# Kernel optimization log

Hardware: AMD Instinct MI355X
Metric: run time of the kernel (lower is better)

## Reference

```python
import jax, jax.numpy as jnp
import numpy as np

N, E = 100000, 800000
DIN, DH, DOUT = 128, 64, 16


def _glorot_linear(k, din, dout):
    s = 1.0 / np.sqrt(din)
    return jax.random.uniform(k, (din, dout), jnp.float32, -s, s)


def setup_inputs() -> dict:
    key = jax.random.key(0)
    ks = jax.random.split(key, 6)
    x = jax.random.normal(ks[0], (N, DIN), jnp.float32)
    edge_index = jax.random.randint(ks[1], (2, E), 0, N, dtype=jnp.int64)
    edge_attr = jax.random.uniform(ks[2], (E,), jnp.float32)  # positive edge weights
    W1 = _glorot_linear(ks[3], DIN, DH)
    b1 = jnp.zeros((DH,), jnp.float32)
    W2 = _glorot_linear(ks[4], DH, DH)
    b2 = jnp.zeros((DH,), jnp.float32)
    W3 = _glorot_linear(ks[5], DH, DOUT)
    b3 = jnp.zeros((DOUT,), jnp.float32)
    return {"x": x, "edge_index": edge_index, "edge_attr": edge_attr,
            "W1": W1, "b1": b1, "W2": W2, "b2": b2, "W3": W3, "b3": b3}


def gcn_conv(x, W, b, src, dst, ew, n):
    """PyG GCNConv: linear transform, add self-loops (weight 1), symmetric
    degree normalization, scatter-add aggregation (source_to_target), bias."""
    h = x @ W                                   # [N, dout]
    deg = jax.ops.segment_sum(ew, dst, num_segments=n) + 1.0  # +1 for self-loop
    dinv = jax.lax.rsqrt(deg)                   # deg >= 1 always
    norm = dinv[src] * ew * dinv[dst]           # [E]
    agg = jax.ops.segment_sum(h[src] * norm[:, None], dst, num_segments=n)
    # self-loop contribution: h[i] * dinv[i]^2
    return agg + h * (dinv * dinv)[:, None] + b


def reference(x, edge_index, edge_attr, W1, b1, W2, b2, W3, b3):
    src, dst = edge_index[0], edge_index[1]
    n = x.shape[0]
    h = jax.nn.relu(gcn_conv(x, W1, b1, src, dst, edge_attr, n))
    # dropout is identity in eval mode
    h = jax.nn.relu(gcn_conv(h, W2, b2, src, dst, edge_attr, n))
    h = gcn_conv(h, W3, b3, src, dst, edge_attr, n)
    return jax.nn.log_softmax(h, axis=1)
```

## Files before the change

### kernel.cpp

```cpp
#include <hip/hip_runtime.h>
#include <hip/hip_bf16.h>
#include <math.h>

#define DIN 128
#define DH 64
#define DOUT_ 16
#define SL 32
#define BSH 9
#define NBMAX 256
#define CAP 5120
#define CH 2048

typedef long long ll;
typedef __attribute__((ext_vector_type(8))) short bf16x8;
typedef __attribute__((ext_vector_type(4))) float f32x4;

__device__ inline ushort f2bf(float f) {
    unsigned u = __float_as_uint(f);
    u += 0x7FFF + ((u >> 16) & 1);
    return (ushort)(u >> 16);
}
__device__ inline float bf2f(ushort s) { return __uint_as_float(((unsigned)s) << 16); }

__global__ __launch_bounds__(256) void bin_and_gemm(const int* __restrict__ src,
                                                    const int* __restrict__ dst,
                                                    const float* __restrict__ ew,
                                                    int* __restrict__ gcur,
                                                    int2* __restrict__ bins, int E,
                                                    const float* __restrict__ X,
                                                    const float* __restrict__ W,
                                                    ushort* __restrict__ H, int N,
                                                    int FB) {
    __shared__ int hist[NBMAX];
    __shared__ int curb[NBMAX];
    __shared__ int baseb[NBMAX];
    __shared__ __align__(16) ushort Wt[DIN * DH];

    const int tid = threadIdx.x;

    if (blockIdx.x < FB) {
        for (int i = tid; i < NBMAX; i += 256) { hist[i] = 0; curb[i] = 0; }
        __syncthreads();
        const int e0 = blockIdx.x * CH;
        const int ecnt = min(E - e0, CH);
        for (int r = tid; r < ecnt; r += 256)
            atomicAdd(&hist[dst[e0 + r] >> BSH], 1);
        __syncthreads();
        for (int b = tid; b < NBMAX; b += 256)
            baseb[b] = hist[b] ? atomicAdd(&gcur[b], hist[b]) : 0;
        __syncthreads();
        for (int r = tid; r < ecnt; r += 256) {
            int e = e0 + r;
            int d = dst[e];
            int b = d >> BSH;
            int off = atomicAdd(&curb[b], 1);
            int pos = baseb[b] + off;
            if (pos < CAP)
                bins[(ll)b * CAP + pos] =
                    make_int2(src[e] | ((d & ((1 << BSH) - 1)) << 20), __float_as_int(ew[e]));
        }
        return;
    }

    const int bid = blockIdx.x - FB;
    for (int f = tid; f < DIN * DH; f += 256) {
        int k = f / DH, c = f % DH;
        Wt[((k >> 3) * DH + c) * 8 + (k & 7)] = f2bf(W[f]);
    }
    __syncthreads();

    const int wave = tid >> 6;
    const int lane = tid & 63;
    const int rowTile = bid * 64 + wave * 16;
    const int arow = rowTile + (lane & 15);
    const int kgrp = lane >> 4;

    f32x4 acc[DH / 16];
    #pragma unroll
    for (int cf = 0; cf < DH / 16; cf++) acc[cf] = (f32x4){0.f, 0.f, 0.f, 0.f};

    #pragma unroll
    for (int ks = 0; ks < DIN / 32; ks++) {
        const int k0 = ks * 32 + kgrp * 8;
        bf16x8 a = {0, 0, 0, 0, 0, 0, 0, 0};
        if (arow < N) {
            const float* xp = X + (ll)arow * DIN + k0;
            float4 f0 = ((const float4*)xp)[0];
            float4 f1 = ((const float4*)xp)[1];
            a[0] = (short)f2bf(f0.x); a[1] = (short)f2bf(f0.y);
            a[2] = (short)f2bf(f0.z); a[3] = (short)f2bf(f0.w);
            a[4] = (short)f2bf(f1.x); a[5] = (short)f2bf(f1.y);
            a[6] = (short)f2bf(f1.z); a[7] = (short)f2bf(f1.w);
        }
        #pragma unroll
        for (int cf = 0; cf < DH / 16; cf++) {
            bf16x8 b = *(const bf16x8*)&Wt[(((k0 >> 3) * DH) + cf * 16 + (lane & 15)) * 8];
            acc[cf] = __builtin_amdgcn_mfma_f32_16x16x32_bf16(a, b, acc[cf], 0, 0, 0);
        }
    }

    const int rbase = rowTile + kgrp * 4;
    #pragma unroll
    for (int cf = 0; cf < DH / 16; cf++) {
        #pragma unroll
        for (int r = 0; r < 4; r++) {
            int row = rbase + r;
            if (row < N)
                H[(ll)row * DH + cf * 16 + (lane & 15)] = f2bf(acc[cf][r]);
        }
    }
}

__global__ __launch_bounds__(256) void debin(const int2* __restrict__ bins,
                                             const int* __restrict__ gcur,
                                             int2* __restrict__ pair, int* __restrict__ cnt,
                                             float* __restrict__ dinv, int N) {
    __shared__ int cl[1 << BSH];
    __shared__ float wsum[1 << BSH];
    const int tid = threadIdx.x;
    for (int i = tid; i < (1 << BSH); i += 256) { cl[i] = 0; wsum[i] = 0.f; }
    __syncthreads();

    const int b = blockIdx.x;
    const int nbase = b << BSH;
    const int m = min(gcur[b], CAP);
    for (int i = tid; i < m; i += 256) {
        int2 t = bins[(ll)b * CAP + i];
        int dlo = t.x >> 20;
        int s = t.x & 0xFFFFF;
        int slot = atomicAdd(&cl[dlo], 1);
        if (slot < SL) pair[(ll)(nbase + dlo) * SL + slot] = make_int2(s, t.y);
        atomicAdd(&wsum[dlo], __int_as_float(t.y));
    }
    __syncthreads();
    for (int i = tid; i < (1 << BSH); i += 256) {
        int node = nbase + i;
        if (node < N) {
            cnt[node] = min(cl[i], SL);
            dinv[node] = rsqrtf(wsum[i] + 1.0f);
        }
    }
}

template <int NC, bool SRC_DINV>
__global__ __launch_bounds__(256) void fused_gg(const ushort* __restrict__ h,
                                                const int2* __restrict__ pair,
                                                const int* __restrict__ cnt,
                                                const float* __restrict__ dinv,
                                                const float* __restrict__ bias,
                                                const float* __restrict__ W,
                                                ushort* __restrict__ Hout, int N) {
    __shared__ __align__(16) ushort Wt[64 * NC];
    __shared__ __align__(16) ushort Hs[64][72];

    for (int f = threadIdx.x; f < 64 * NC; f += 256) {
        int k = f / NC, c = f % NC;
        Wt[((k >> 3) * NC + c) * 8 + (k & 7)] = f2bf(W[f]);
    }

    const int tid = threadIdx.x;
    const int grp = tid >> 4;
    const int l16 = tid & 15;
    const ushort4* h4 = (const ushort4*)h;

    #pragma unroll
    for (int pass = 0; pass < 4; pass++) {
        int nl = pass * 16 + grp;
        int node = blockIdx.x * 64 + nl;
        float4 acc = make_float4(0.f, 0.f, 0.f, 0.f);
        float di = 0.f;
        float hx = 0.f, hy = 0.f, hz = 0.f, hw = 0.f;
        float4 bv = make_float4(0.f, 0.f, 0.f, 0.f);
        if (node < N) {
            int deg = min(cnt[node], SL);
            const int2* p = pair + (ll)node * SL;
            int e = 0;
            for (; e + 1 < deg; e += 2) {
                int2 p0 = p[e];
                int2 p1 = p[e + 1];
                ushort4 a0 = h4[(ll)p0.x * 16 + l16];
                ushort4 a1 = h4[(ll)p1.x * 16 + l16];
                float w0 = __int_as_float(p0.y);
                float w1 = __int_as_float(p1.y);
                if (SRC_DINV) { w0 *= dinv[p0.x]; w1 *= dinv[p1.x]; }
                acc.x += bf2f(a0.x) * w0 + bf2f(a1.x) * w1;
                acc.y += bf2f(a0.y) * w0 + bf2f(a1.y) * w1;
                acc.z += bf2f(a0.z) * w0 + bf2f(a1.z) * w1;
                acc.w += bf2f(a0.w) * w0 + bf2f(a1.w) * w1;
            }
            if (e < deg) {
                int2 pp = p[e];
                ushort4 a0 = h4[(ll)pp.x * 16 + l16];
                float w = __int_as_float(pp.y);
                if (SRC_DINV) w *= dinv[pp.x];
                acc.x += bf2f(a0.x) * w;
                acc.y += bf2f(a0.y) * w;
                acc.z += bf2f(a0.z) * w;
                acc.w += bf2f(a0.w) * w;
            }
            di = dinv[node];
            ushort4 hs = h4[(ll)node * 16 + l16];
            float sf = SRC_DINV ? di : 1.0f;
            hx = bf2f(hs.x) * sf; hy = bf2f(hs.y) * sf;
            hz = bf2f(hs.z) * sf; hw = bf2f(hs.w) * sf;
            bv = ((const float4*)bias)[l16];
        }
        float rx = fmaxf(di * (acc.x + hx) + bv.x, 0.f);
        float ry = fmaxf(di * (acc.y + hy) + bv.y, 0.f);
        float rz = fmaxf(di * (acc.z + hz) + bv.z, 0.f);
        float rw = fmaxf(di * (acc.w + hw) + bv.w, 0.f);
        *(ushort4*)&Hs[nl][l16 * 4] = make_ushort4(f2bf(rx), f2bf(ry), f2bf(rz), f2bf(rw));
    }
    __syncthreads();

    const int wave = tid >> 6;
    const int lane = tid & 63;
    const int kgrp = lane >> 4;
    f32x4 acc2[NC / 16];
    #pragma unroll
    for (int cf = 0; cf < NC / 16; cf++) acc2[cf] = (f32x4){0.f, 0.f, 0.f, 0.f};

    #pragma unroll
    for (int ks = 0; ks < 2; ks++) {
        const int k0 = ks * 32 + kgrp * 8;
        bf16x8 a = *(const bf16x8*)&Hs[wave * 16 + (lane & 15)][k0];
        #pragma unroll
        for (int cf = 0; cf < NC / 16; cf++) {
            bf16x8 b = *(const bf16x8*)&Wt[(((k0 >> 3) * NC) + cf * 16 + (lane & 15)) * 8];
            acc2[cf] = __builtin_amdgcn_mfma_f32_16x16x32_bf16(a, b, acc2[cf], 0, 0, 0);
        }
    }

    const int rbase = blockIdx.x * 64 + wave * 16 + kgrp * 4;
    float dsc[4];
    #pragma unroll
    for (int r = 0; r < 4; r++) dsc[r] = (rbase + r < N) ? dinv[rbase + r] : 1.0f;
    #pragma unroll
    for (int cf = 0; cf < NC / 16; cf++) {
        #pragma unroll
        for (int r = 0; r < 4; r++) {
            int row = rbase + r;
            if (row < N)
                Hout[(ll)row * NC + cf * 16 + (lane & 15)] = f2bf(acc2[cf][r] * dsc[r]);
        }
    }
}

__global__ __launch_bounds__(256) void gather16_final(const ushort* __restrict__ h3,
                                                      const int2* __restrict__ pair,
                                                      const int* __restrict__ cnt,
                                                      const float* __restrict__ dinv,
                                                      const float* __restrict__ b3,
                                                      float* __restrict__ out, int N) {
    int node = blockIdx.x * 32 + (threadIdx.x >> 3);
    int lane = threadIdx.x & 7;
    if (node >= N) return;
    int deg = min(cnt[node], SL);
    const int2* p = pair + (ll)node * SL;

    const ushort2* h2 = (const ushort2*)h3;
    float ax = 0.f, ay = 0.f;
    int e = 0;
    for (; e + 1 < deg; e += 2) {
        int2 p0 = p[e];
        int2 p1 = p[e + 1];
        ushort2 a0 = h2[(ll)p0.x * 8 + lane];
        ushort2 a1 = h2[(ll)p1.x * 8 + lane];
        float w0 = __int_as_float(p0.y);
        float w1 = __int_as_float(p1.y);
        ax += bf2f(a0.x) * w0 + bf2f(a1.x) * w1;
        ay += bf2f(a0.y) * w0 + bf2f(a1.y) * w1;
    }
    if (e < deg) {
        int2 pp = p[e];
        ushort2 a0 = h2[(ll)pp.x * 8 + lane];
        float w = __int_as_float(pp.y);
        ax += bf2f(a0.x) * w;
        ay += bf2f(a0.y) * w;
    }

    float di = dinv[node];
    ushort2 hs = h2[(ll)node * 8 + lane];
    float zx = di * (ax + bf2f(hs.x)) + b3[lane * 2];
    float zy = di * (ay + bf2f(hs.y)) + b3[lane * 2 + 1];

    float m = fmaxf(zx, zy);
    #pragma unroll
    for (int o = 4; o; o >>= 1) m = fmaxf(m, __shfl_xor(m, o, 8));
    float s = expf(zx - m) + expf(zy - m);
    #pragma unroll
    for (int o = 4; o; o >>= 1) s += __shfl_xor(s, o, 8);
    float l = logf(s);
    float2 r;
    r.x = zx - m - l;
    r.y = zy - m - l;
    ((float2*)out)[(ll)node * 8 + lane] = r;
}

extern "C" void kernel_launch(void* const* d_in, const int* in_sizes, int n_in,
                              void* d_out, int out_size, void* d_ws, size_t ws_size,
                              hipStream_t stream) {
    const float* x = (const float*)d_in[0];
    const int* ei = (const int*)d_in[1];
    const float* ew = (const float*)d_in[2];
    const float* W1 = (const float*)d_in[3];
    const float* b1 = (const float*)d_in[4];
    const float* W2 = (const float*)d_in[5];
    const float* b2 = (const float*)d_in[6];
    const float* W3 = (const float*)d_in[7];
    const float* b3 = (const float*)d_in[8];

    const int N = in_sizes[0] / DIN;
    const int E = in_sizes[2];
    const int* src = ei;
    const int* dst = ei + E;

    float* out = (float*)d_out;

    int2* pair = (int2*)d_ws;
    ushort* A = (ushort*)(pair + (ll)N * SL);
    ushort* A2 = A + (ll)N * DH;
    ushort* C = A2 + (ll)N * DH;
    float* dinv = (float*)(C + (ll)N * DOUT_);
    int* cnt = (int*)(dinv + N);
    int* gcur = cnt + N;
    int2* bins = (int2*)A2;

    const int TB = 256;
    const int NB = (N + (1 << BSH) - 1) >> BSH;
    const int FB = (E + CH - 1) / CH;
    const int rowBlocks = (N + 63) / 64;

    hipMemsetAsync(gcur, 0, NBMAX * sizeof(int), stream);
    bin_and_gemm<<<FB + rowBlocks, TB, 0, stream>>>(src, dst, ew, gcur, bins, E,
                                                    x, W1, A, N, FB);
    debin<<<NB, TB, 0, stream>>>(bins, gcur, pair, cnt, dinv, N);

    fused_gg<DH, true><<<rowBlocks, TB, 0, stream>>>(A, pair, cnt, dinv, b1, W2, A2, N);

    fused_gg<DOUT_, false><<<rowBlocks, TB, 0, stream>>>(A2, pair, cnt, dinv, b2, W3, C, N);

    gather16_final<<<(N + 31) / 32, TB, 0, stream>>>(C, pair, cnt, dinv, b3, out, N);
}
```

Measured before the change: 127.2 us.

## Enlarge binning chunk, widen debin blocks, unroll gather loops by four

Raises the edge chunk per binning block from 2048 to 8192, which reduces the number of binning blocks and their atomic contention on the global bin cursors. The debin kernel now runs with 512 threads per block so each bin is processed with more parallelism. The neighbor-gather loops in fused_gg and gather16_final are unrolled by four instead of two, putting more independent loads in flight. Larger chunks mean fewer binning blocks, which may leave the GPU less occupied during binning.

```diff
diff --git a/kernel.cpp b/kernel.cpp
--- a/kernel.cpp
+++ b/kernel.cpp
@@ -9,7 +9,7 @@
 #define BSH 9
 #define NBMAX 256
 #define CAP 5120
-#define CH 2048
+#define CH 8192
 
 typedef long long ll;
 typedef __attribute__((ext_vector_type(8))) short bf16x8;
@@ -111,20 +111,20 @@
     }
 }
 
-__global__ __launch_bounds__(256) void debin(const int2* __restrict__ bins,
+__global__ __launch_bounds__(512) void debin(const int2* __restrict__ bins,
                                              const int* __restrict__ gcur,
                                              int2* __restrict__ pair, int* __restrict__ cnt,
                                              float* __restrict__ dinv, int N) {
     __shared__ int cl[1 << BSH];
     __shared__ float wsum[1 << BSH];
     const int tid = threadIdx.x;
-    for (int i = tid; i < (1 << BSH); i += 256) { cl[i] = 0; wsum[i] = 0.f; }
+    for (int i = tid; i < (1 << BSH); i += 512) { cl[i] = 0; wsum[i] = 0.f; }
     __syncthreads();
 
     const int b = blockIdx.x;
     const int nbase = b << BSH;
     const int m = min(gcur[b], CAP);
-    for (int i = tid; i < m; i += 256) {
+    for (int i = tid; i < m; i += 512) {
         int2 t = bins[(ll)b * CAP + i];
         int dlo = t.x >> 20;
         int s = t.x & 0xFFFFF;
@@ -133,7 +133,7 @@
         atomicAdd(&wsum[dlo], __int_as_float(t.y));
     }
     __syncthreads();
-    for (int i = tid; i < (1 << BSH); i += 256) {
+    for (int i = tid; i < (1 << BSH); i += 512) {
         int node = nbase + i;
         if (node < N) {
             cnt[node] = min(cl[i], SL);
@@ -175,20 +175,29 @@
             int deg = min(cnt[node], SL);
             const int2* p = pair + (ll)node * SL;
             int e = 0;
-            for (; e + 1 < deg; e += 2) {
+            for (; e + 3 < deg; e += 4) {
                 int2 p0 = p[e];
                 int2 p1 = p[e + 1];
+                int2 p2 = p[e + 2];
+                int2 p3 = p[e + 3];
                 ushort4 a0 = h4[(ll)p0.x * 16 + l16];
                 ushort4 a1 = h4[(ll)p1.x * 16 + l16];
+                ushort4 a2 = h4[(ll)p2.x * 16 + l16];
+                ushort4 a3 = h4[(ll)p3.x * 16 + l16];
                 float w0 = __int_as_float(p0.y);
                 float w1 = __int_as_float(p1.y);
-                if (SRC_DINV) { w0 *= dinv[p0.x]; w1 *= dinv[p1.x]; }
-                acc.x += bf2f(a0.x) * w0 + bf2f(a1.x) * w1;
-                acc.y += bf2f(a0.y) * w0 + bf2f(a1.y) * w1;
-                acc.z += bf2f(a0.z) * w0 + bf2f(a1.z) * w1;
-                acc.w += bf2f(a0.w) * w0 + bf2f(a1.w) * w1;
+                float w2 = __int_as_float(p2.y);
+                float w3 = __int_as_float(p3.y);
+                if (SRC_DINV) {
+                    w0 *= dinv[p0.x]; w1 *= dinv[p1.x];
+                    w2 *= dinv[p2.x]; w3 *= dinv[p3.x];
+                }
+                acc.x += bf2f(a0.x) * w0 + bf2f(a1.x) * w1 + bf2f(a2.x) * w2 + bf2f(a3.x) * w3;
+                acc.y += bf2f(a0.y) * w0 + bf2f(a1.y) * w1 + bf2f(a2.y) * w2 + bf2f(a3.y) * w3;
+                acc.z += bf2f(a0.z) * w0 + bf2f(a1.z) * w1 + bf2f(a2.z) * w2 + bf2f(a3.z) * w3;
+                acc.w += bf2f(a0.w) * w0 + bf2f(a1.w) * w1 + bf2f(a2.w) * w2 + bf2f(a3.w) * w3;
             }
-            if (e < deg) {
+            for (; e < deg; e++) {
                 int2 pp = p[e];
                 ushort4 a0 = h4[(ll)pp.x * 16 + l16];
                 float w = __int_as_float(pp.y);
@@ -261,17 +270,23 @@
     const ushort2* h2 = (const ushort2*)h3;
     float ax = 0.f, ay = 0.f;
     int e = 0;
-    for (; e + 1 < deg; e += 2) {
+    for (; e + 3 < deg; e += 4) {
         int2 p0 = p[e];
         int2 p1 = p[e + 1];
+        int2 p2 = p[e + 2];
+        int2 p3 = p[e + 3];
         ushort2 a0 = h2[(ll)p0.x * 8 + lane];
         ushort2 a1 = h2[(ll)p1.x * 8 + lane];
+        ushort2 a2 = h2[(ll)p2.x * 8 + lane];
+        ushort2 a3 = h2[(ll)p3.x * 8 + lane];
         float w0 = __int_as_float(p0.y);
         float w1 = __int_as_float(p1.y);
-        ax += bf2f(a0.x) * w0 + bf2f(a1.x) * w1;
-        ay += bf2f(a0.y) * w0 + bf2f(a1.y) * w1;
-    }
-    if (e < deg) {
+        float w2 = __int_as_float(p2.y);
+        float w3 = __int_as_float(p3.y);
+        ax += bf2f(a0.x) * w0 + bf2f(a1.x) * w1 + bf2f(a2.x) * w2 + bf2f(a3.x) * w3;
+        ay += bf2f(a0.y) * w0 + bf2f(a1.y) * w1 + bf2f(a2.y) * w2 + bf2f(a3.y) * w3;
+    }
+    for (; e < deg; e++) {
         int2 pp = p[e];
         ushort2 a0 = h2[(ll)pp.x * 8 + lane];
         float w = __int_as_float(pp.y);
@@ -334,7 +349,7 @@
     hipMemsetAsync(gcur, 0, NBMAX * sizeof(int), stream);
     bin_and_gemm<<<FB + rowBlocks, TB, 0, stream>>>(src, dst, ew, gcur, bins, E,
                                                     x, W1, A, N, FB);
-    debin<<<NB, TB, 0, stream>>>(bins, gcur, pair, cnt, dinv, N);
+    debin<<<NB, 512, 0, stream>>>(bins, gcur, pair, cnt, dinv, N);
 
     fused_gg<DH, true><<<rowBlocks, TB, 0, stream>>>(A, pair, cnt, dinv, b1, W2, A2, N);
 
```

New measurement: 128.8 us. About the same (+1.3%).
